# Performance work log

Hardware: AMD Instinct MI355X
Metric: run time of the kernel (lower is better)

Reference implementation:

```python
import jax, jax.numpy as jnp
import numpy as np

R = 4
D = 2 * R + 1  # 9
B, C, H, W = 1, 256, 48, 96


def setup_inputs() -> dict:
    key = jax.random.key(0)
    k1, k2, k3, k4, k5 = jax.random.split(key, 5)
    f1 = jax.random.normal(k1, (B, C, H, W), dtype=jnp.float32)
    f2 = jax.random.normal(k2, (B, C, H, W), dtype=jnp.float32)
    cx = jax.random.uniform(k3, (B, H, W), dtype=jnp.float32) * (W - 1)
    cy = jax.random.uniform(k4, (B, H, W), dtype=jnp.float32) * (H - 1)
    coords = jnp.stack([cx, cy], axis=1)  # (B,2,H,W), ch0=x, ch1=y
    # DAP: 1x1 conv over (2r+1)^2 channels, identity init (perturbed so it is non-trivial)
    w_dap = jnp.eye(D * D, dtype=jnp.float32) + 0.02 * jax.random.normal(k5, (D * D, D * D), dtype=jnp.float32)
    return {"f1": f1, "f2": f2, "coords": coords, "w_dap": w_dap}


def _bilinear_sample(img, px, py):
    # img: (C,H,W); px,py: (M,) pixel coords; zeros padding, align_corners=True semantics
    c, h, w = img.shape
    x0 = jnp.floor(px)
    y0 = jnp.floor(py)
    x1 = x0 + 1.0
    y1 = y0 + 1.0
    wx1 = px - x0
    wx0 = 1.0 - wx1
    wy1 = py - y0
    wy0 = 1.0 - wy1
    flat = img.reshape(c, h * w)

    def corner(xi, yi, wgt):
        valid = (xi >= 0) & (xi <= w - 1) & (yi >= 0) & (yi <= h - 1)
        xc = jnp.clip(xi, 0, w - 1).astype(jnp.int32)
        yc = jnp.clip(yi, 0, h - 1).astype(jnp.int32)
        v = flat[:, yc * w + xc]  # (C,M)
        return v * (wgt * valid.astype(wgt.dtype))[None, :]

    return (corner(x0, y0, wx0 * wy0) + corner(x1, y0, wx1 * wy0)
            + corner(x0, y1, wx0 * wy1) + corner(x1, y1, wx1 * wy1))


def _corr_forward(f1, f2, coords, w_dap):
    b, c, h, w = f1.shape
    d = jnp.linspace(-R, R, D, dtype=f1.dtype)
    # centroids[b, i, y, j, x] = (coords_x + dx[i], coords_y + dy[j])
    px = coords[:, 0][:, None, :, None, :] + d[None, :, None, None, None]  # (B,D,H,1,W)->(B,D,H,D,W)
    py = coords[:, 1][:, None, :, None, :] + d[None, None, None, :, None]
    px = jnp.broadcast_to(px, (b, D, h, D, w)).reshape(b, -1)
    py = jnp.broadcast_to(py, (b, D, h, D, w)).reshape(b, -1)
    samp = jax.vmap(_bilinear_sample)(f2, px, py)  # (B, C, D*H*D*W)
    f2s = samp.reshape(b, c, D, h, D, w)
    corr = jnp.einsum('bcihjw,bchw->bijhw', f2s, f1) / jnp.sqrt(jnp.asarray(c, f1.dtype))
    cf = corr.reshape(b, D * D, h, w)
    out = jnp.einsum('od,bdhw->bohw', w_dap, cf)  # DAP 1x1 conv, no bias
    return out  # (B, (2r+1)^2, H, W)


def reference(f1, f2, coords, w_dap):
    return _corr_forward(f1, f2, coords, w_dap)
```

## Files before the change

kernel.cpp:

```cpp
#include <hip/hip_runtime.h>

#define HH   48
#define WW   96
#define CC   256
#define DD   9
#define DD2  81
#define HWSZ (HH * WW)
#define ROWB 512
#define ZOFF ((unsigned)HWSZ * ROWB)
#define NCX  24
#define NCY  24
#define NCELL (NCX * NCY)
#define HROWS 143
#define HRP   144
#define HROWB 256
#define CAP  32

typedef __attribute__((ext_vector_type(8))) short short8v;
typedef __attribute__((ext_vector_type(4))) float f32x4;

__device__ __forceinline__ unsigned bf16rne(float f) {
  unsigned u = __float_as_uint(f);
  return (u + 0x7FFFu + ((u >> 16) & 1u)) >> 16;
}

__device__ __forceinline__ void gload_lds16(const char* g, char* l) {
  __builtin_amdgcn_global_load_lds(
      (const __attribute__((address_space(1))) char*)g,
      (__attribute__((address_space(3))) char*)l, 16, 0, 0);
}

__global__ __launch_bounds__(256) void transpose_to_bf16(
    const float* __restrict__ f1, const float* __restrict__ f2,
    const float* __restrict__ w_dap, const float* __restrict__ coords,
    char* __restrict__ f2tb, char* __restrict__ f1tb, char* __restrict__ zpage,
    unsigned short* __restrict__ Wf, int* __restrict__ cnt,
    int* __restrict__ plist) {
  __shared__ float tile[64][65];
  const float* src = (blockIdx.y == 0) ? f1 : f2;
  char* dst = (blockIdx.y == 0) ? f1tb : f2tb;

  const int tid = threadIdx.x;
  if (blockIdx.y == 0 && blockIdx.x == 0 && tid < 32) {
    float4 z = {0.f, 0.f, 0.f, 0.f};
    *(float4*)(zpage + tid * 16) = z;
  }
  if (blockIdx.y == 0 && blockIdx.x < 36) {
    int gid = blockIdx.x * 256 + tid;
    int g = gid >> 9;
    int idx = gid & 511;
    int ln = idx >> 3, e = idx & 7;
    int m = g / 3, kt = g - m * 3;
    int r = m * 16 + (ln & 15);
    int c = kt * 32 + (ln >> 4) * 8 + e;
    float v = (r < DD2 && c < DD2) ? w_dap[r * DD2 + c] : 0.f;
    Wf[gid] = (unsigned short)bf16rne(v);
  }
  if (blockIdx.y == 1 && blockIdx.x < 18) {
    const int p = blockIdx.x * 256 + tid;
    const int ix = (int)coords[p];
    const int iy = (int)coords[HWSZ + p];
    const int cell = (iy >> 1) * NCX + (ix >> 2);
    const int slot = atomicAdd(&cnt[cell], 1);
    if (slot < CAP) plist[cell * CAP + slot] = p;
  }

  const int tiles_p = HWSZ / 64;
  const int bc = blockIdx.x / tiles_p;
  const int bp = blockIdx.x % tiles_p;
  const int c0 = bc * 64, p0 = bp * 64;

#pragma unroll
  for (int k = 0; k < 16; k++) {
    int idx = k * 256 + tid;
    int cl = idx >> 6, pl = idx & 63;
    tile[cl][pl] = src[(size_t)(c0 + cl) * HWSZ + p0 + pl];
  }
  __syncthreads();
#pragma unroll
  for (int k = 0; k < 8; k++) {
    int idx = k * 256 + tid;
    int pl = idx >> 5, cp = idx & 31;
    unsigned lo = bf16rne(tile[2 * cp][pl]);
    unsigned hi = bf16rne(tile[2 * cp + 1][pl]);
    *(unsigned*)(dst + (size_t)(p0 + pl) * ROWB + (size_t)c0 * 2 + cp * 4) =
        lo | (hi << 16);
  }
}

__global__ __launch_bounds__(256, 3) void corr_region(
    const char* __restrict__ f2tb, const char* __restrict__ f1tb,
    const float* __restrict__ coords, const int* __restrict__ cnt,
    const int* __restrict__ plist, unsigned short* __restrict__ cbg) {
  __shared__ __align__(16) char halo[HRP * HROWB];
  __shared__ float dsf[HRP * 16];
  __shared__ unsigned rowoff[HRP];

  const int cell = blockIdx.x;
  const int ci = cell % NCX, cj = cell / NCX;
  const int npix0 = cnt[cell];
  const int npix = npix0 < CAP ? npix0 : CAP;
  if (npix == 0) return;

  const int tid = threadIdx.x;
  const int lane = tid & 63, wid = tid >> 6;
  const int hi = lane >> 4, lo = lane & 15;

  const int hx0 = ci * 4 - 4, hy0 = cj * 2 - 4;

  if (tid < HRP) {
    unsigned ro = ZOFF;
    if (tid < HROWS) {
      const int hy = (tid * 158) >> 11;
      const int hx = tid - hy * 13;
      const int gy = hy0 + hy, gx = hx0 + hx;
      if (gx >= 0 && gx < WW && gy >= 0 && gy < HH)
        ro = (unsigned)(gy * WW + gx) * ROWB;
    }
    rowoff[tid] = ro;
  }
  __syncthreads();

  const int nb = (npix + 15) >> 4;
  for (int b = 0; b < nb; ++b) {
    const int slot = b * 16 + lo;
    const bool valid = slot < npix;
    const int pi = valid ? plist[cell * CAP + slot] : 0;
    const char* fb = valid ? (f1tb + (size_t)pi * ROWB) : (f2tb + ZOFF);
    short8v bq[8];
#pragma unroll
    for (int kt = 0; kt < 8; kt++)
      bq[kt] = *(const short8v*)(fb + kt * 64 + hi * 16);

    f32x4 acc0 = {0.f, 0.f, 0.f, 0.f};
    f32x4 acc1 = {0.f, 0.f, 0.f, 0.f};
    f32x4 acc2 = {0.f, 0.f, 0.f, 0.f};

#pragma unroll
    for (int pass = 0; pass < 2; pass++) {
      for (int s = wid; s < 36; s += 4) {
        const int r = 4 * s + hi;
        gload_lds16(
            f2tb + rowoff[r] + pass * 256 + ((lo * 16) ^ ((r & 7) << 4)),
            &halo[s * 1024]);
      }
      __syncthreads();

      {
        const int rr = wid * 16 + lo;
        const int swz = (rr & 7) << 4;
        const char* rp = halo + rr * HROWB;
        short8v a0 = *(const short8v*)(rp + ((hi * 16 + 0) ^ swz));
        short8v a1 = *(const short8v*)(rp + ((hi * 16 + 64) ^ swz));
        short8v a2 = *(const short8v*)(rp + ((hi * 16 + 128) ^ swz));
        short8v a3 = *(const short8v*)(rp + ((hi * 16 + 192) ^ swz));
        acc0 = __builtin_amdgcn_mfma_f32_16x16x32_bf16(a0, bq[pass * 4 + 0], acc0, 0, 0, 0);
        acc0 = __builtin_amdgcn_mfma_f32_16x16x32_bf16(a1, bq[pass * 4 + 1], acc0, 0, 0, 0);
        acc0 = __builtin_amdgcn_mfma_f32_16x16x32_bf16(a2, bq[pass * 4 + 2], acc0, 0, 0, 0);
        acc0 = __builtin_amdgcn_mfma_f32_16x16x32_bf16(a3, bq[pass * 4 + 3], acc0, 0, 0, 0);
      }
      {
        const int rr = (wid + 4) * 16 + lo;
        const int swz = (rr & 7) << 4;
        const char* rp = halo + rr * HROWB;
        short8v a0 = *(const short8v*)(rp + ((hi * 16 + 0) ^ swz));
        short8v a1 = *(const short8v*)(rp + ((hi * 16 + 64) ^ swz));
        short8v a2 = *(const short8v*)(rp + ((hi * 16 + 128) ^ swz));
        short8v a3 = *(const short8v*)(rp + ((hi * 16 + 192) ^ swz));
        acc1 = __builtin_amdgcn_mfma_f32_16x16x32_bf16(a0, bq[pass * 4 + 0], acc1, 0, 0, 0);
        acc1 = __builtin_amdgcn_mfma_f32_16x16x32_bf16(a1, bq[pass * 4 + 1], acc1, 0, 0, 0);
        acc1 = __builtin_amdgcn_mfma_f32_16x16x32_bf16(a2, bq[pass * 4 + 2], acc1, 0, 0, 0);
        acc1 = __builtin_amdgcn_mfma_f32_16x16x32_bf16(a3, bq[pass * 4 + 3], acc1, 0, 0, 0);
      }
      if (wid == 0) {
        const int rr = 8 * 16 + lo;
        const int swz = (rr & 7) << 4;
        const char* rp = halo + rr * HROWB;
        short8v a0 = *(const short8v*)(rp + ((hi * 16 + 0) ^ swz));
        short8v a1 = *(const short8v*)(rp + ((hi * 16 + 64) ^ swz));
        short8v a2 = *(const short8v*)(rp + ((hi * 16 + 128) ^ swz));
        short8v a3 = *(const short8v*)(rp + ((hi * 16 + 192) ^ swz));
        acc2 = __builtin_amdgcn_mfma_f32_16x16x32_bf16(a0, bq[pass * 4 + 0], acc2, 0, 0, 0);
        acc2 = __builtin_amdgcn_mfma_f32_16x16x32_bf16(a1, bq[pass * 4 + 1], acc2, 0, 0, 0);
        acc2 = __builtin_amdgcn_mfma_f32_16x16x32_bf16(a2, bq[pass * 4 + 2], acc2, 0, 0, 0);
        acc2 = __builtin_amdgcn_mfma_f32_16x16x32_bf16(a3, bq[pass * 4 + 3], acc2, 0, 0, 0);
      }
      __syncthreads();
    }

#pragma unroll
    for (int j = 0; j < 4; j++)
      dsf[(wid * 16 + hi * 4 + j) * 16 + lo] = acc0[j];
#pragma unroll
    for (int j = 0; j < 4; j++)
      dsf[((wid + 4) * 16 + hi * 4 + j) * 16 + lo] = acc1[j];
    if (wid == 0) {
#pragma unroll
      for (int j = 0; j < 4; j++)
        dsf[(8 * 16 + hi * 4 + j) * 16 + lo] = acc2[j];
    }
    __syncthreads();

    {
      const int s2 = tid & 15;
      const int g = tid >> 4;
      const int slot2 = b * 16 + s2;
      if (slot2 < npix) {
        const int pi2 = plist[cell * CAP + slot2];
        const float cx = coords[pi2];
        const float cy = coords[HWSZ + pi2];
        const float fxf = floorf(cx), fyf = floorf(cy);
        const float fx = cx - fxf, fy = cy - fyf;
        const int ox = (int)fxf - ci * 4;
        const int oy = (int)fyf - cj * 2;
#pragma unroll
        for (int e = 0; e < 6; e++) {
          const int o = g * 6 + e;
          if (o < DD2) {
            const int i = o / DD, j = o - i * DD;
            const int rb = (oy + j) * 13 + ox + i;
            const float d00 = dsf[rb * 16 + s2];
            const float d01 = dsf[(rb + 1) * 16 + s2];
            const float d10 = dsf[(rb + 13) * 16 + s2];
            const float d11 = dsf[(rb + 14) * 16 + s2];
            const float c = (1.f - fy) * ((1.f - fx) * d00 + fx * d01) +
                            fy * ((1.f - fx) * d10 + fx * d11);
            cbg[(size_t)pi2 * 96 + o] = (unsigned short)bf16rne(c * 0.0625f);
          }
        }
      }
    }
    if (b + 1 < nb) __syncthreads();
  }
}

__global__ __launch_bounds__(64) void dap_gemm(
    const unsigned short* __restrict__ cbg, const unsigned short* __restrict__ Wf,
    float* __restrict__ out) {
  const int lane = threadIdx.x;
  const int hi = lane >> 4, lo = lane & 15;
  const int p0 = blockIdx.x * 16;

  short8v bq[3];
#pragma unroll
  for (int kt = 0; kt < 3; kt++)
    bq[kt] = *(const short8v*)(cbg + (size_t)(p0 + lo) * 96 + kt * 32 + hi * 8);

  f32x4 acc[6];
#pragma unroll
  for (int m = 0; m < 6; m++) acc[m] = (f32x4){0.f, 0.f, 0.f, 0.f};

#pragma unroll
  for (int m = 0; m < 6; m++) {
#pragma unroll
    for (int kt = 0; kt < 3; kt++) {
      short8v aw = *(const short8v*)(Wf + ((size_t)(m * 3 + kt) * 64 + lane) * 8);
      acc[m] = __builtin_amdgcn_mfma_f32_16x16x32_bf16(aw, bq[kt], acc[m], 0, 0, 0);
    }
  }

#pragma unroll
  for (int m = 0; m < 6; m++) {
#pragma unroll
    for (int j = 0; j < 4; j++) {
      const int o = m * 16 + hi * 4 + j;
      if (o < DD2) out[(size_t)o * HWSZ + p0 + lo] = acc[m][j];
    }
  }
}

extern "C" void kernel_launch(void* const* d_in, const int* in_sizes, int n_in,
                              void* d_out, int out_size, void* d_ws, size_t ws_size,
                              hipStream_t stream) {
  const float* f1     = (const float*)d_in[0];
  const float* f2     = (const float*)d_in[1];
  const float* coords = (const float*)d_in[2];
  const float* w_dap  = (const float*)d_in[3];
  float* out = (float*)d_out;

  char* f2tb  = (char*)d_ws;
  char* zpage = f2tb + (size_t)HWSZ * ROWB;
  char* f1tb  = zpage + 512;
  unsigned short* Wf  = (unsigned short*)(f1tb + (size_t)HWSZ * ROWB);
  unsigned short* cbg = Wf + 9216;
  int* cnt   = (int*)((char*)cbg + (size_t)HWSZ * 96 * 2);
  int* plist = cnt + NCELL;

  hipMemsetAsync(cnt, 0, NCELL * sizeof(int), stream);

  dim3 tgrid((CC / 64) * (HWSZ / 64), 2);
  transpose_to_bf16<<<tgrid, 256, 0, stream>>>(f1, f2, w_dap, coords, f2tb, f1tb,
                                               zpage, Wf, cnt, plist);

  corr_region<<<dim3(NCELL), 256, 0, stream>>>(f2tb, f1tb, coords, cnt, plist, cbg);

  dap_gemm<<<dim3(HWSZ / 16), 64, 0, stream>>>(cbg, Wf, out);
}
```

Baseline: 31.01 us.

## Fuse DAP 1x1-conv GEMM into corr_region epilogue via LDS staging

Removes the separate dap_gemm kernel and the global cbg intermediate buffer. Each 16-pixel batch of correlation values is now written as bf16 into a padded LDS tile, and the MFMA 1x1 conv runs inside corr_region, scattering results straight to the output. This drops one kernel launch and a global round trip of the correlation volume. In exchange it adds a block barrier per batch, extra LDS use that may lower occupancy, and output writes scattered by pixel index rather than contiguous.

```diff
diff --git a/kernel.cpp b/kernel.cpp
--- a/kernel.cpp
+++ b/kernel.cpp
@@ -15,6 +15,7 @@
 #define HRP   144
 #define HROWB 256
 #define CAP  32
+#define CBL_STR 104
 
 typedef __attribute__((ext_vector_type(8))) short short8v;
 typedef __attribute__((ext_vector_type(4))) float f32x4;
@@ -91,10 +92,12 @@
 __global__ __launch_bounds__(256, 3) void corr_region(
     const char* __restrict__ f2tb, const char* __restrict__ f1tb,
     const float* __restrict__ coords, const int* __restrict__ cnt,
-    const int* __restrict__ plist, unsigned short* __restrict__ cbg) {
+    const int* __restrict__ plist, const unsigned short* __restrict__ Wf,
+    float* __restrict__ out) {
   __shared__ __align__(16) char halo[HRP * HROWB];
   __shared__ float dsf[HRP * 16];
   __shared__ unsigned rowoff[HRP];
+  __shared__ __align__(16) unsigned short cbl[16 * CBL_STR];
 
   const int cell = blockIdx.x;
   const int ci = cell % NCX, cj = cell / NCX;
@@ -216,6 +219,7 @@
 #pragma unroll
         for (int e = 0; e < 6; e++) {
           const int o = g * 6 + e;
+          float cv = 0.f;
           if (o < DD2) {
             const int i = o / DD, j = o - i * DD;
             const int rb = (oy + j) * 13 + ox + i;
@@ -223,49 +227,44 @@
             const float d01 = dsf[(rb + 1) * 16 + s2];
             const float d10 = dsf[(rb + 13) * 16 + s2];
             const float d11 = dsf[(rb + 14) * 16 + s2];
-            const float c = (1.f - fy) * ((1.f - fx) * d00 + fx * d01) +
-                            fy * ((1.f - fx) * d10 + fx * d11);
-            cbg[(size_t)pi2 * 96 + o] = (unsigned short)bf16rne(c * 0.0625f);
+            cv = ((1.f - fy) * ((1.f - fx) * d00 + fx * d01) +
+                  fy * ((1.f - fx) * d10 + fx * d11)) * 0.0625f;
+          }
+          cbl[s2 * CBL_STR + o] = (unsigned short)bf16rne(cv);
+        }
+      }
+    }
+    __syncthreads();
+
+    {
+      short8v bq2[3];
+#pragma unroll
+      for (int kt = 0; kt < 3; kt++)
+        bq2[kt] = *(const short8v*)&cbl[lo * CBL_STR + kt * 32 + hi * 8];
+      const int slot3 = b * 16 + lo;
+      const bool v3 = slot3 < npix;
+      const int po = v3 ? plist[cell * CAP + slot3] : 0;
+#pragma unroll
+      for (int mi = 0; mi < 2; mi++) {
+        const int m = wid + mi * 4;
+        if (m < 6) {
+          f32x4 acc = {0.f, 0.f, 0.f, 0.f};
+#pragma unroll
+          for (int kt = 0; kt < 3; kt++) {
+            short8v aw = *(const short8v*)(Wf + ((size_t)(m * 3 + kt) * 64 + lane) * 8);
+            acc = __builtin_amdgcn_mfma_f32_16x16x32_bf16(aw, bq2[kt], acc, 0, 0, 0);
+          }
+          if (v3) {
+#pragma unroll
+            for (int j = 0; j < 4; j++) {
+              const int o = m * 16 + hi * 4 + j;
+              if (o < DD2) out[(size_t)o * HWSZ + po] = acc[j];
+            }
           }
         }
       }
     }
     if (b + 1 < nb) __syncthreads();
-  }
-}
-
-__global__ __launch_bounds__(64) void dap_gemm(
-    const unsigned short* __restrict__ cbg, const unsigned short* __restrict__ Wf,
-    float* __restrict__ out) {
-  const int lane = threadIdx.x;
-  const int hi = lane >> 4, lo = lane & 15;
-  const int p0 = blockIdx.x * 16;
-
-  short8v bq[3];
-#pragma unroll
-  for (int kt = 0; kt < 3; kt++)
-    bq[kt] = *(const short8v*)(cbg + (size_t)(p0 + lo) * 96 + kt * 32 + hi * 8);
-
-  f32x4 acc[6];
-#pragma unroll
-  for (int m = 0; m < 6; m++) acc[m] = (f32x4){0.f, 0.f, 0.f, 0.f};
-
-#pragma unroll
-  for (int m = 0; m < 6; m++) {
-#pragma unroll
-    for (int kt = 0; kt < 3; kt++) {
-      short8v aw = *(const short8v*)(Wf + ((size_t)(m * 3 + kt) * 64 + lane) * 8);
-      acc[m] = __builtin_amdgcn_mfma_f32_16x16x32_bf16(aw, bq[kt], acc[m], 0, 0, 0);
-    }
-  }
-
-#pragma unroll
-  for (int m = 0; m < 6; m++) {
-#pragma unroll
-    for (int j = 0; j < 4; j++) {
-      const int o = m * 16 + hi * 4 + j;
-      if (o < DD2) out[(size_t)o * HWSZ + p0 + lo] = acc[m][j];
-    }
   }
 }
 
@@ -281,9 +280,8 @@
   char* f2tb  = (char*)d_ws;
   char* zpage = f2tb + (size_t)HWSZ * ROWB;
   char* f1tb  = zpage + 512;
-  unsigned short* Wf  = (unsigned short*)(f1tb + (size_t)HWSZ * ROWB);
-  unsigned short* cbg = Wf + 9216;
-  int* cnt   = (int*)((char*)cbg + (size_t)HWSZ * 96 * 2);
+  unsigned short* Wf = (unsigned short*)(f1tb + (size_t)HWSZ * ROWB);
+  int* cnt   = (int*)(Wf + 9216);
   int* plist = cnt + NCELL;
 
   hipMemsetAsync(cnt, 0, NCELL * sizeof(int), stream);
@@ -292,7 +290,5 @@
   transpose_to_bf16<<<tgrid, 256, 0, stream>>>(f1, f2, w_dap, coords, f2tb, f1tb,
                                                zpage, Wf, cnt, plist);
 
-  corr_region<<<dim3(NCELL), 256, 0, stream>>>(f2tb, f1tb, coords, cnt, plist, cbg);
-
-  dap_gemm<<<dim3(HWSZ / 16), 64, 0, stream>>>(cbg, Wf, out);
-}
+  corr_region<<<dim3(NCELL), 256, 0, stream>>>(f2tb, f1tb, coords, cnt, plist, Wf, out);
+}
```

After: 29.64 us. 1.05x faster.
